# Optimization experiments

Measured on AMD Instinct MI355X. Metric: run time of the kernel, lower is better.

## Reference

```python
import jax, jax.numpy as jnp
from jax import lax
import numpy as np

# Dcls2_1d config (matches init_kwargs)
K_H, K_W = 3, 3          # base kernel size
DIL = 4                  # max dilation along dim 0 (learnable spacings)
LIM = DIL // 2           # each tap may move +/- LIM rows
KH_EFF = K_H + 2 * LIM   # constructed kernel height (7)
PAD_H = 1 + LIM          # user padding 1 adjusted by dilation//2 (as in _adjust_padding)
PAD_W = 1


def build_kernel(weight, P1):
    """Construct dense conv kernel by bilinear scatter of weights at
    continuous learnable row offsets P1. weight,P1: (O, I, K_H, K_W).
    Returns (O, I, KH_EFF, K_W)."""
    kh = jnp.arange(K_H, dtype=weight.dtype)[None, None, :, None]
    pos = kh + LIM + jnp.clip(P1, -LIM, LIM)      # continuous row position in [0, KH_EFF-1]
    p0 = jnp.floor(pos)
    frac = pos - p0                                # interpolation residual (grad flows to P)
    p0i = p0.astype(jnp.int32)
    oh0 = jax.nn.one_hot(p0i, KH_EFF, dtype=weight.dtype)        # (O,I,Kh,Kw,KH_EFF)
    oh1 = jax.nn.one_hot(p0i + 1, KH_EFF, dtype=weight.dtype)    # OOB rows -> all-zero row
    return (jnp.einsum('oihw,oihwk->oikw', weight * (1.0 - frac), oh0)
            + jnp.einsum('oihw,oihwk->oikw', weight * frac, oh1))


def setup_inputs() -> dict:
    key = jax.random.key(0)
    k1, k2, k3, k4 = jax.random.split(key, 4)
    x = jax.random.normal(k1, (16, 128, 64, 64), jnp.float32)
    weight = jax.random.normal(k2, (256, 128, 3, 3), jnp.float32) * 0.03
    bias = jax.random.normal(k3, (256,), jnp.float32) * 0.01
    # learnable positions span the allowed +/- LIM range to exercise interpolation
    P = jax.random.uniform(k4, (1, 256, 128, 3, 3), jnp.float32, -2.0, 2.0)
    return {"x": x, "weight": weight, "bias": bias, "P": P}


def reference(x, weight, bias, P):
    K = build_kernel(weight, P[0])
    out = lax.conv_general_dilated(
        x, K,
        window_strides=(1, 1),
        padding=((PAD_H, PAD_H), (PAD_W, PAD_W)),
        dimension_numbers=('NCHW', 'OIHW', 'NCHW'),
        feature_group_count=1)
    return out + bias[None, :, None, None]
```

## Files before the change

kernel.cpp:

```cpp
#include <hip/hip_runtime.h>
#include <hip/hip_bf16.h>

#define NIMG 16
#define CIN 128
#define COUT 256
#define HH 64
#define WW 64
#define KHE 7
#define KW_ 3
#define HP (HH + 6)
#define WP (WW + 2)
#define KDIM (CIN * KHE * KW_)
#define NKT 42
#define NKSLICE (NKT * 2)

typedef __attribute__((ext_vector_type(8))) short short8;
typedef __attribute__((ext_vector_type(4))) float f32x4;

#define AS1(p) ((const __attribute__((address_space(1))) void*)(p))
#define AS3(p) ((__attribute__((address_space(3))) void*)(p))

__global__ void __launch_bounds__(256) pad_convert(const float* __restrict__ x,
                                                   ushort* __restrict__ xp) {
  const int bid = blockIdx.x;
  const int n = bid / HP, hp = bid % HP;
  const int h = hp - 3;
  ushort* dst = xp + (size_t)(n * HP + hp) * (WP * CIN);
  const int tid = threadIdx.x;

  if (h < 0 || h >= HH) {
    uint4* p = (uint4*)dst;
    uint4 z; z.x = z.y = z.z = z.w = 0u;
    for (int idx = tid; idx < (WP * CIN * 2) / 16; idx += 256) p[idx] = z;
    return;
  }

  __shared__ ushort t[CIN][WW + 1];
  for (int it = 0; it < (CIN * WW) / 256; ++it) {
    int flat = it * 256 + tid;
    int i = flat >> 6, w = flat & 63;
    float v = x[(((size_t)n * CIN + i) * HH + h) * WW + w];
    __hip_bfloat16 b = __float2bfloat16(v);
    t[i][w] = *(ushort*)&b;
  }
  __syncthreads();
  for (int it = 0; it < (WP * CIN) / 256; ++it) {
    int flat = it * 256 + tid;
    int wp = flat >> 7, i = flat & 127;
    int w = wp - 1;
    ushort v = (w < 0 || w >= WW) ? (ushort)0 : t[i][w];
    dst[flat] = v;
  }
}

__global__ void __launch_bounds__(256) build_kb(const float* __restrict__ weight,
                                                const float* __restrict__ P,
                                                ushort* __restrict__ kb2) {
  int idx = blockIdx.x * 256 + threadIdx.x;
  if (idx >= COUT * KW_ * CIN) return;
  int i = idx & 127;
  int kw = (idx >> 7) % 3;
  int o = idx / (KW_ * CIN);
  int base = (o * CIN + i) * 9 + kw;

  float a[KHE] = {0.f, 0.f, 0.f, 0.f, 0.f, 0.f, 0.f};
#pragma unroll
  for (int kh = 0; kh < 3; ++kh) {
    float wv = weight[base + kh * 3];
    float p = P[base + kh * 3];
    p = fminf(2.f, fmaxf(-2.f, p));
    float pos = (float)(kh + 2) + p;
    float fl = floorf(pos);
    float fr = pos - fl;
    int r0 = (int)fl;
    float c0 = wv * (1.f - fr);
    float c1 = wv * fr;
#pragma unroll
    for (int r = 0; r < KHE; ++r) {
      a[r] += ((r0 == r) ? c0 : 0.f) + ((r0 + 1 == r) ? c1 : 0.f);
    }
  }
#pragma unroll
  for (int r = 0; r < KHE; ++r) {
    __hip_bfloat16 b = __float2bfloat16(a[r]);
    int kslice = (r * 3 + kw) * 4 + (i >> 5);
    kb2[(size_t)kslice * 8192 + o * 32 + (i & 31)] = *(ushort*)&b;
  }
}

__global__ void __launch_bounds__(512, 2) dcls_gemm(const ushort* __restrict__ xp,
                                                    const ushort* __restrict__ kb2,
                                                    const float* __restrict__ bias,
                                                    float* __restrict__ out) {
  __shared__ __align__(16) ushort As[2][256 * 64];

  const int tid = threadIdx.x;
  const int lane = tid & 63;
  const int wv = tid >> 6;
  const int wr = wv >> 2;
  const int wc = wv & 3;
  const int g = lane >> 4;
  const int lm = lane & 15;
  const int m0 = blockIdx.x << 8;

  const int srow = tid >> 3;
  const int swz = ((tid & 7) ^ (srow & 7)) * 8;

  const ushort* pA[4];
#pragma unroll
  for (int j = 0; j < 4; ++j) {
    int r = j * 64 + srow;
    int m = m0 + r;
    int ni = m >> 12, hh = (m >> 6) & 63, ww = m & 63;
    pA[j] = xp + (size_t)((ni * HP + hh) * WP + ww) * CIN + swz;
  }

  const ushort* kbB = kb2 + (size_t)wc * 2048 + lm * 32 + g * 8;

#define STAGEA(c, kt) do { \
    int kh_ = (kt) / 6; int rem_ = (kt) - kh_ * 6; \
    int kw2_ = rem_ >> 1; int ic_ = rem_ & 1; \
    int offA_ = (kh_ * WP + kw2_) * CIN + ic_ * 64; \
    _Pragma("unroll") \
    for (int j_ = 0; j_ < 4; ++j_) \
      __builtin_amdgcn_global_load_lds(AS1(pA[j_] + offA_), AS3(&As[c][(j_ * 64 + wv * 8) * 64]), 16, 0, 0); \
  } while (0)

#define LOADB(dst, kt) do { \
    _Pragma("unroll") \
    for (int n_ = 0; n_ < 4; ++n_) \
      _Pragma("unroll") \
      for (int kk_ = 0; kk_ < 2; ++kk_) \
        dst[n_][kk_] = *(const short8*)(kbB + (size_t)((kt) * 2 + kk_) * 8192 + n_ * 512); \
  } while (0)

  f32x4 acc[8][4] = {};
  const int swzR = (lm & 7) << 4;

  short8 bf0[4][2], bf1[4][2];

#define TILE_MFMA(c, bf) do { \
    const char* Ab = (const char*)&As[c][0]; \
    _Pragma("unroll") \
    for (int half_ = 0; half_ < 2; ++half_) { \
      short8 af[4][2]; \
      _Pragma("unroll") \
      for (int m4_ = 0; m4_ < 4; ++m4_) \
        _Pragma("unroll") \
        for (int kk_ = 0; kk_ < 2; ++kk_) { \
          int rowA_ = wr * 128 + half_ * 64 + m4_ * 16 + lm; \
          af[m4_][kk_] = *(const short8*)(Ab + rowA_ * 128 + ((kk_ * 64 + g * 16) ^ swzR)); \
        } \
      _Pragma("unroll") \
      for (int kk_ = 0; kk_ < 2; ++kk_) \
        _Pragma("unroll") \
        for (int m4_ = 0; m4_ < 4; ++m4_) \
          _Pragma("unroll") \
          for (int n_ = 0; n_ < 4; ++n_) \
            acc[half_ * 4 + m4_][n_] = __builtin_amdgcn_mfma_f32_16x16x32_bf16( \
                af[m4_][kk_], bf[n_][kk_], acc[half_ * 4 + m4_][n_], 0, 0, 0); \
    } \
  } while (0)

#define SUBITER(kt, c, bfc) do { \
    asm volatile("s_waitcnt vmcnt(12)" ::: "memory"); \
    __builtin_amdgcn_s_barrier(); \
    __builtin_amdgcn_sched_barrier(0); \
    TILE_MFMA(c, bfc); \
    int ktn_ = ((kt) + 2 < NKT) ? (kt) + 2 : 0; \
    LOADB(bfc, ktn_); \
    __builtin_amdgcn_s_barrier(); \
    __builtin_amdgcn_sched_barrier(0); \
    STAGEA(c, ktn_); \
  } while (0)

  STAGEA(0, 0);
  LOADB(bf0, 0);
  STAGEA(1, 1);
  LOADB(bf1, 1);

  for (int kt = 0; kt < NKT; kt += 2) {
    SUBITER(kt, 0, bf0);
    SUBITER(kt + 1, 1, bf1);
  }
#undef SUBITER
#undef TILE_MFMA
#undef LOADB
#undef STAGEA

#pragma unroll
  for (int fn = 0; fn < 4; ++fn) {
    int o = wc * 64 + fn * 16 + lm;
    float bv = bias[o];
#pragma unroll
    for (int fm = 0; fm < 8; ++fm) {
      int m = m0 + wr * 128 + fm * 16 + g * 4;
      int ni = m >> 12, hh = (m >> 6) & 63, ww = m & 63;
      f32x4 v = acc[fm][fn];
      v[0] += bv; v[1] += bv; v[2] += bv; v[3] += bv;
      *(f32x4*)(out + (size_t)((ni * COUT + o) * HH + hh) * WW + ww) = v;
    }
  }
}

extern "C" void kernel_launch(void* const* d_in, const int* in_sizes, int n_in,
                              void* d_out, int out_size, void* d_ws, size_t ws_size,
                              hipStream_t stream) {
  const float* x = (const float*)d_in[0];
  const float* weight = (const float*)d_in[1];
  const float* bias = (const float*)d_in[2];
  const float* P = (const float*)d_in[3];
  float* out = (float*)d_out;

  const size_t xp_elems = (size_t)NIMG * HP * WP * CIN;
  ushort* xp = (ushort*)d_ws;
  ushort* kb2 = (ushort*)((char*)d_ws + xp_elems * 2);

  hipLaunchKernelGGL(pad_convert, dim3(NIMG * HP), dim3(256), 0, stream, x, xp);
  hipLaunchKernelGGL(build_kb, dim3((COUT * KW_ * CIN + 255) / 256), dim3(256), 0, stream,
                     weight, P, kb2);
  hipLaunchKernelGGL(dcls_gemm, dim3(65536 / 256), dim3(512), 0, stream, xp, kb2, bias, out);
}
```

Baseline: 99.55 us.

## Switch GEMM to 32x32x16 MFMA with 4-stage LDS ring and new layouts

The implicit-GEMM kernel now uses 32x32x16 bf16 MFMA instead of 16x16x32. The weight layout is reorganized into 8-element k-slices, and the A tile in LDS becomes a k-major layout without XOR swizzle. The LDS buffer grows to four stages, so the next stage's async global-to-LDS load is issued before the current tile's MFMAs and one of the two barriers per subiteration is dropped. This aims to cut LDS read traffic per FLOP and barrier overhead. It raises LDS usage to 128KB per block, which may limit occupancy to one block per CU despite launch bounds of 2, and may introduce LDS bank conflicts.

```diff
diff --git a/kernel.cpp b/kernel.cpp
--- a/kernel.cpp
+++ b/kernel.cpp
@@ -12,10 +12,10 @@
 #define WP (WW + 2)
 #define KDIM (CIN * KHE * KW_)
 #define NKT 42
-#define NKSLICE (NKT * 2)
 
 typedef __attribute__((ext_vector_type(8))) short short8;
 typedef __attribute__((ext_vector_type(4))) float f32x4;
+typedef __attribute__((ext_vector_type(16))) float f32x16;
 
 #define AS1(p) ((const __attribute__((address_space(1))) void*)(p))
 #define AS3(p) ((__attribute__((address_space(3))) void*)(p))
@@ -83,8 +83,8 @@
 #pragma unroll
   for (int r = 0; r < KHE; ++r) {
     __hip_bfloat16 b = __float2bfloat16(a[r]);
-    int kslice = (r * 3 + kw) * 4 + (i >> 5);
-    kb2[(size_t)kslice * 8192 + o * 32 + (i & 31)] = *(ushort*)&b;
+    int ks = (r * 3 + kw) * 16 + (i >> 3);
+    kb2[(size_t)ks * 2048 + o * 8 + (i & 7)] = *(ushort*)&b;
   }
 }
 
@@ -92,86 +92,71 @@
                                                     const ushort* __restrict__ kb2,
                                                     const float* __restrict__ bias,
                                                     float* __restrict__ out) {
-  __shared__ __align__(16) ushort As[2][256 * 64];
+  __shared__ __align__(16) ushort As[4][16384];
 
   const int tid = threadIdx.x;
   const int lane = tid & 63;
   const int wv = tid >> 6;
   const int wr = wv >> 2;
   const int wc = wv & 3;
-  const int g = lane >> 4;
-  const int lm = lane & 15;
   const int m0 = blockIdx.x << 8;
 
-  const int srow = tid >> 3;
-  const int swz = ((tid & 7) ^ (srow & 7)) * 8;
-
   const ushort* pA[4];
 #pragma unroll
   for (int j = 0; j < 4; ++j) {
-    int r = j * 64 + srow;
-    int m = m0 + r;
+    int m = m0 + j * 64 + lane;
     int ni = m >> 12, hh = (m >> 6) & 63, ww = m & 63;
-    pA[j] = xp + (size_t)((ni * HP + hh) * WP + ww) * CIN + swz;
-  }
-
-  const ushort* kbB = kb2 + (size_t)wc * 2048 + lm * 32 + g * 8;
-
-#define STAGEA(c, kt) do { \
-    int kh_ = (kt) / 6; int rem_ = (kt) - kh_ * 6; \
-    int kw2_ = rem_ >> 1; int ic_ = rem_ & 1; \
+    pA[j] = xp + (size_t)((ni * HP + hh) * WP + ww) * CIN + wv * 8;
+  }
+  const ushort* kbB = kb2 + (size_t)(lane >> 5) * 2048 + (size_t)(wc * 64 + (lane & 31)) * 8;
+
+#define STAGEA(buf, kt) do { \
+    int kh_ = (kt) / 6, rem_ = (kt) - kh_ * 6, kw2_ = rem_ >> 1, ic_ = rem_ & 1; \
     int offA_ = (kh_ * WP + kw2_) * CIN + ic_ * 64; \
     _Pragma("unroll") \
     for (int j_ = 0; j_ < 4; ++j_) \
-      __builtin_amdgcn_global_load_lds(AS1(pA[j_] + offA_), AS3(&As[c][(j_ * 64 + wv * 8) * 64]), 16, 0, 0); \
+      __builtin_amdgcn_global_load_lds(AS1(pA[j_] + offA_), \
+          AS3((char*)&As[buf][0] + wv * 4096 + j_ * 1024), 16, 0, 0); \
   } while (0)
 
 #define LOADB(dst, kt) do { \
     _Pragma("unroll") \
-    for (int n_ = 0; n_ < 4; ++n_) \
+    for (int n_ = 0; n_ < 2; ++n_) \
       _Pragma("unroll") \
-      for (int kk_ = 0; kk_ < 2; ++kk_) \
-        dst[n_][kk_] = *(const short8*)(kbB + (size_t)((kt) * 2 + kk_) * 8192 + n_ * 512); \
-  } while (0)
-
-  f32x4 acc[8][4] = {};
-  const int swzR = (lm & 7) << 4;
-
-  short8 bf0[4][2], bf1[4][2];
-
-#define TILE_MFMA(c, bf) do { \
-    const char* Ab = (const char*)&As[c][0]; \
+      for (int kk_ = 0; kk_ < 4; ++kk_) \
+        dst[n_][kk_] = *(const short8*)(kbB + ((size_t)((kt) * 8 + kk_ * 2) * 2048 + n_ * 256)); \
+  } while (0)
+
+  f32x16 acc[4][2] = {};
+  short8 bf0[2][4], bf1[2][4];
+
+#define TILE_MFMA(buf, bfc) do { \
+    const char* Ab = (const char*)&As[buf][0]; \
     _Pragma("unroll") \
-    for (int half_ = 0; half_ < 2; ++half_) { \
-      short8 af[4][2]; \
+    for (int mf_ = 0; mf_ < 4; ++mf_) { \
+      short8 af[4]; \
       _Pragma("unroll") \
-      for (int m4_ = 0; m4_ < 4; ++m4_) \
+      for (int kk_ = 0; kk_ < 4; ++kk_) \
+        af[kk_] = *(const short8*)(Ab + kk_ * 8192 + (lane >> 5) * 4096 + \
+                                   (wr * 128 + mf_ * 32 + (lane & 31)) * 16); \
+      _Pragma("unroll") \
+      for (int kk_ = 0; kk_ < 4; ++kk_) \
         _Pragma("unroll") \
-        for (int kk_ = 0; kk_ < 2; ++kk_) { \
-          int rowA_ = wr * 128 + half_ * 64 + m4_ * 16 + lm; \
-          af[m4_][kk_] = *(const short8*)(Ab + rowA_ * 128 + ((kk_ * 64 + g * 16) ^ swzR)); \
-        } \
-      _Pragma("unroll") \
-      for (int kk_ = 0; kk_ < 2; ++kk_) \
-        _Pragma("unroll") \
-        for (int m4_ = 0; m4_ < 4; ++m4_) \
-          _Pragma("unroll") \
-          for (int n_ = 0; n_ < 4; ++n_) \
-            acc[half_ * 4 + m4_][n_] = __builtin_amdgcn_mfma_f32_16x16x32_bf16( \
-                af[m4_][kk_], bf[n_][kk_], acc[half_ * 4 + m4_][n_], 0, 0, 0); \
+        for (int n_ = 0; n_ < 2; ++n_) \
+          acc[mf_][n_] = __builtin_amdgcn_mfma_f32_32x32x16_bf16( \
+              af[kk_], bfc[n_][kk_], acc[mf_][n_], 0, 0, 0); \
     } \
   } while (0)
 
-#define SUBITER(kt, c, bfc) do { \
+#define SUBITER(kt, bfc) do { \
+    __builtin_amdgcn_sched_barrier(0); \
     asm volatile("s_waitcnt vmcnt(12)" ::: "memory"); \
     __builtin_amdgcn_s_barrier(); \
     __builtin_amdgcn_sched_barrier(0); \
-    TILE_MFMA(c, bfc); \
-    int ktn_ = ((kt) + 2 < NKT) ? (kt) + 2 : 0; \
-    LOADB(bfc, ktn_); \
-    __builtin_amdgcn_s_barrier(); \
-    __builtin_amdgcn_sched_barrier(0); \
-    STAGEA(c, ktn_); \
+    { int ktn_ = ((kt) + 2 < NKT) ? (kt) + 2 : 0; \
+      STAGEA(((kt) + 2) & 3, ktn_); \
+      TILE_MFMA((kt) & 3, bfc); \
+      LOADB(bfc, ktn_); } \
   } while (0)
 
   STAGEA(0, 0);
@@ -180,8 +165,8 @@
   LOADB(bf1, 1);
 
   for (int kt = 0; kt < NKT; kt += 2) {
-    SUBITER(kt, 0, bf0);
-    SUBITER(kt + 1, 1, bf1);
+    SUBITER(kt, bf0);
+    SUBITER(kt + 1, bf1);
   }
 #undef SUBITER
 #undef TILE_MFMA
@@ -189,16 +174,30 @@
 #undef STAGEA
 
 #pragma unroll
-  for (int fn = 0; fn < 4; ++fn) {
-    int o = wc * 64 + fn * 16 + lm;
+  for (int n_ = 0; n_ < 2; ++n_)
+#pragma unroll
+    for (int kk_ = 0; kk_ < 4; ++kk_) {
+      asm volatile("" :: "v"((int)bf0[n_][kk_][0]));
+      asm volatile("" :: "v"((int)bf1[n_][kk_][0]));
+    }
+
+#pragma unroll
+  for (int nf = 0; nf < 2; ++nf) {
+    int o = wc * 64 + nf * 32 + (lane & 31);
     float bv = bias[o];
 #pragma unroll
-    for (int fm = 0; fm < 8; ++fm) {
-      int m = m0 + wr * 128 + fm * 16 + g * 4;
-      int ni = m >> 12, hh = (m >> 6) & 63, ww = m & 63;
-      f32x4 v = acc[fm][fn];
-      v[0] += bv; v[1] += bv; v[2] += bv; v[3] += bv;
-      *(f32x4*)(out + (size_t)((ni * COUT + o) * HH + hh) * WW + ww) = v;
+    for (int mf = 0; mf < 4; ++mf) {
+#pragma unroll
+      for (int q = 0; q < 4; ++q) {
+        int m = m0 + wr * 128 + mf * 32 + q * 8 + (lane >> 5) * 4;
+        int ni = m >> 12, hh = (m >> 6) & 63, ww = m & 63;
+        f32x4 v;
+        v[0] = acc[mf][nf][q * 4 + 0] + bv;
+        v[1] = acc[mf][nf][q * 4 + 1] + bv;
+        v[2] = acc[mf][nf][q * 4 + 2] + bv;
+        v[3] = acc[mf][nf][q * 4 + 3] + bv;
+        *(f32x4*)(out + (size_t)((ni * COUT + o) * HH + hh) * WW + ww) = v;
+      }
     }
   }
 }
```

Result: slower. 116.5 us (+17.0%).

## Quad-buffer LDS A tiles and drop one barrier per GEMM sub-iteration

Applied to the files above, without the earlier changes.

The shared-memory A staging grows from two to four buffers, so the tile for step kt+2 goes into a buffer no wave is still reading. The asynchronous global-to-LDS load can then be issued before the MFMA work for step kt rather than after it, and the second block barrier per sub-iteration is removed. Dummy asm uses keep the B fragment registers live past the loop. LDS use per block rises to 128KB, which rules out two resident blocks per CU, but the grid of 256 blocks already gives roughly one block per CU.

```diff
diff --git a/kernel.cpp b/kernel.cpp
--- a/kernel.cpp
+++ b/kernel.cpp
@@ -12,7 +12,6 @@
 #define WP (WW + 2)
 #define KDIM (CIN * KHE * KW_)
 #define NKT 42
-#define NKSLICE (NKT * 2)
 
 typedef __attribute__((ext_vector_type(8))) short short8;
 typedef __attribute__((ext_vector_type(4))) float f32x4;
@@ -92,7 +91,7 @@
                                                     const ushort* __restrict__ kb2,
                                                     const float* __restrict__ bias,
                                                     float* __restrict__ out) {
-  __shared__ __align__(16) ushort As[2][256 * 64];
+  __shared__ __align__(16) ushort As[4][256 * 64];
 
   const int tid = threadIdx.x;
   const int lane = tid & 63;
@@ -117,13 +116,13 @@
 
   const ushort* kbB = kb2 + (size_t)wc * 2048 + lm * 32 + g * 8;
 
-#define STAGEA(c, kt) do { \
+#define STAGEA(buf, kt) do { \
     int kh_ = (kt) / 6; int rem_ = (kt) - kh_ * 6; \
     int kw2_ = rem_ >> 1; int ic_ = rem_ & 1; \
     int offA_ = (kh_ * WP + kw2_) * CIN + ic_ * 64; \
     _Pragma("unroll") \
     for (int j_ = 0; j_ < 4; ++j_) \
-      __builtin_amdgcn_global_load_lds(AS1(pA[j_] + offA_), AS3(&As[c][(j_ * 64 + wv * 8) * 64]), 16, 0, 0); \
+      __builtin_amdgcn_global_load_lds(AS1(pA[j_] + offA_), AS3(&As[buf][(j_ * 64 + wv * 8) * 64]), 16, 0, 0); \
   } while (0)
 
 #define LOADB(dst, kt) do { \
@@ -139,8 +138,8 @@
 
   short8 bf0[4][2], bf1[4][2];
 
-#define TILE_MFMA(c, bf) do { \
-    const char* Ab = (const char*)&As[c][0]; \
+#define TILE_MFMA(buf, bf) do { \
+    const char* Ab = (const char*)&As[buf][0]; \
     _Pragma("unroll") \
     for (int half_ = 0; half_ < 2; ++half_) { \
       short8 af[4][2]; \
@@ -162,16 +161,15 @@
     } \
   } while (0)
 
-#define SUBITER(kt, c, bfc) do { \
+#define SUBITER(kt, bfc) do { \
+    __builtin_amdgcn_sched_barrier(0); \
     asm volatile("s_waitcnt vmcnt(12)" ::: "memory"); \
     __builtin_amdgcn_s_barrier(); \
     __builtin_amdgcn_sched_barrier(0); \
-    TILE_MFMA(c, bfc); \
-    int ktn_ = ((kt) + 2 < NKT) ? (kt) + 2 : 0; \
-    LOADB(bfc, ktn_); \
-    __builtin_amdgcn_s_barrier(); \
-    __builtin_amdgcn_sched_barrier(0); \
-    STAGEA(c, ktn_); \
+    { int ktn_ = ((kt) + 2 < NKT) ? (kt) + 2 : 0; \
+      STAGEA(((kt) + 2) & 3, ktn_); \
+      TILE_MFMA((kt) & 3, bfc); \
+      LOADB(bfc, ktn_); } \
   } while (0)
 
   STAGEA(0, 0);
@@ -180,13 +178,21 @@
   LOADB(bf1, 1);
 
   for (int kt = 0; kt < NKT; kt += 2) {
-    SUBITER(kt, 0, bf0);
-    SUBITER(kt + 1, 1, bf1);
+    SUBITER(kt, bf0);
+    SUBITER(kt + 1, bf1);
   }
 #undef SUBITER
 #undef TILE_MFMA
 #undef LOADB
 #undef STAGEA
+
+#pragma unroll
+  for (int n_ = 0; n_ < 4; ++n_)
+#pragma unroll
+    for (int kk_ = 0; kk_ < 2; ++kk_) {
+      asm volatile("" :: "v"((int)bf0[n_][kk_][0]));
+      asm volatile("" :: "v"((int)bf1[n_][kk_][0]));
+    }
 
 #pragma unroll
   for (int fn = 0; fn < 4; ++fn) {
```

After: 96.74 us. -2.8%, faster.
